# Optimization experiments

Measured on AMD Instinct MI355X. Metric: run time of the kernel, lower is better.

Reference implementation:

```python
import jax, jax.numpy as jnp
import numpy as np

N, E, D, H, L = 20000, 320000, 128, 8, 3
C = D // H  # per-head channels = 16


def setup_inputs() -> dict:
    key = jax.random.key(0)
    ks = jax.random.split(key, 20)
    s = 1.0 / np.sqrt(D)
    inp = {
        "x": jax.random.normal(ks[0], (N, D), dtype=jnp.float32),
        "edge_index": jax.random.randint(ks[1], (2, E), 0, N, dtype=jnp.int64),
        "Wq": jax.random.normal(ks[2], (L, D, D), dtype=jnp.float32) * s,
        "bq": jnp.zeros((L, D), dtype=jnp.float32),
        "Wk": jax.random.normal(ks[3], (L, D, D), dtype=jnp.float32) * s,
        "bk": jnp.zeros((L, D), dtype=jnp.float32),
        "Wv": jax.random.normal(ks[4], (L, D, D), dtype=jnp.float32) * s,
        "bv": jnp.zeros((L, D), dtype=jnp.float32),
        "Wskip": jax.random.normal(ks[5], (L, D, D), dtype=jnp.float32) * s,
        "bskip": jnp.zeros((L, D), dtype=jnp.float32),
        "Wbeta": jax.random.normal(ks[6], (L, 3 * D, 1), dtype=jnp.float32) * (1.0 / np.sqrt(3 * D)),
        "ln_g": jnp.ones((L, D), dtype=jnp.float32),
        "ln_b": jnp.zeros((L, D), dtype=jnp.float32),
        "Wout": jax.random.normal(ks[7], (D, D), dtype=jnp.float32) * s,
        "bout": jnp.zeros((D,), dtype=jnp.float32),
    }
    return inp


def _layer_norm(x, g, b, eps=1e-5):
    mu = jnp.mean(x, axis=-1, keepdims=True)
    var = jnp.mean(jnp.square(x - mu), axis=-1, keepdims=True)
    return (x - mu) * jax.lax.rsqrt(var + eps) * g + b


def _transformer_conv(x, src, dst, Wq, bq, Wk, bk, Wv, bv, Wskip, bskip, Wbeta):
    # project q/k/v: [N, D] -> [N, H, C]
    q = (x @ Wq + bq).reshape(N, H, C)
    k = (x @ Wk + bk).reshape(N, H, C)
    v = (x @ Wv + bv).reshape(N, H, C)
    # per-edge attention logits: [E, H]
    alpha = jnp.sum(q[dst] * k[src], axis=-1) / np.sqrt(C)
    # scatter-softmax over edges grouped by dst node
    m = jax.ops.segment_max(alpha, dst, num_segments=N)  # [N, H]
    m = jnp.where(jnp.isfinite(m), m, 0.0)
    ea = jnp.exp(alpha - m[dst])
    denom = jax.ops.segment_sum(ea, dst, num_segments=N)  # [N, H]
    attn = ea / (denom[dst] + 1e-16)  # [E, H]
    # weighted message aggregation: [N, H, C] -> [N, D]
    out = jax.ops.segment_sum(attn[:, :, None] * v[src], dst, num_segments=N)
    out = out.reshape(N, D)
    # beta-gated skip connection (beta=True, root_weight=True)
    x_r = x @ Wskip + bskip
    beta = jax.nn.sigmoid(jnp.concatenate([out, x_r, out - x_r], axis=-1) @ Wbeta)  # [N, 1]
    return beta * x_r + (1.0 - beta) * out


def reference(x, edge_index, Wq, bq, Wk, bk, Wv, bv, Wskip, bskip, Wbeta, ln_g, ln_b, Wout, bout):
    src, dst = edge_index[0], edge_index[1]
    for i in range(L):
        residual = x
        x = _transformer_conv(x, src, dst, Wq[i], bq[i], Wk[i], bk[i], Wv[i], bv[i],
                              Wskip[i], bskip[i], Wbeta[i])
        x = jax.nn.relu(x)  # dropout is identity in eval mode
        x = _layer_norm(x + residual, ln_g[i], ln_b[i])
    return x @ Wout + bout
```

## Files before the change

### kernel.cpp

```cpp
#include <hip/hip_runtime.h>

#define N_NODES 20000
#define N_EDGES 320000
#define DIM 128
#define NLAYER 3
#define SCAN_BLK 1024
#define N_SCAN_BLKS ((N_NODES + SCAN_BLK - 1) / SCAN_BLK)

typedef __attribute__((ext_vector_type(8))) short short8;
typedef __attribute__((ext_vector_type(4))) float f32x4;

__device__ inline ushort f2bf(float f) {
  uint u = __float_as_uint(f);
  uint r = (u + 0x7fffu + ((u >> 16) & 1u)) >> 16;
  return (ushort)r;
}
__device__ inline float bf2f(ushort u) { return __uint_as_float(((uint)u) << 16); }


__global__ void zero_ints_kernel(int* __restrict__ p, int n) {
  int i = blockIdx.x * 256 + threadIdx.x;
  if (i < n) p[i] = 0;
}

__global__ void count_deg_kernel(const int* __restrict__ ei, int* __restrict__ deg) {
  int e = blockIdx.x * 256 + threadIdx.x;
  if (e < N_EDGES) atomicAdd(&deg[ei[N_EDGES + e]], 1);
}

__global__ __launch_bounds__(SCAN_BLK) void scan1_kernel(const int* __restrict__ deg,
                                                         int* __restrict__ rowptr,
                                                         int* __restrict__ blksum) {
  __shared__ int wsum[16];
  int t = threadIdx.x, lane = t & 63, w = t >> 6;
  int i = blockIdx.x * SCAN_BLK + t;
  int val = (i < N_NODES) ? deg[i] : 0;
  int s = val;
  #pragma unroll
  for (int off = 1; off < 64; off <<= 1) {
    int u = __shfl_up(s, off);
    if (lane >= off) s += u;
  }
  if (lane == 63) wsum[w] = s;
  __syncthreads();
  if (t < 16) {
    int wv = wsum[t];
    int ss = wv;
    #pragma unroll
    for (int off = 1; off < 16; off <<= 1) {
      int u = __shfl_up(ss, off);
      if (t >= off) ss += u;
    }
    wsum[t] = ss - wv;
  }
  __syncthreads();
  int excl = wsum[w] + s - val;
  if (i < N_NODES) rowptr[i] = excl;
  if (t == SCAN_BLK - 1) blksum[blockIdx.x] = excl + val;
}

__global__ void scan2_kernel(int* __restrict__ blksum, int* __restrict__ rowptr) {
  int t = threadIdx.x;
  int val = (t < N_SCAN_BLKS) ? blksum[t] : 0;
  int s = val;
  #pragma unroll
  for (int off = 1; off < 64; off <<= 1) {
    int u = __shfl_up(s, off);
    if (t >= off) s += u;
  }
  if (t < N_SCAN_BLKS) blksum[t] = s - val;
  if (t == 63) rowptr[N_NODES] = s;
}

__global__ __launch_bounds__(SCAN_BLK) void scan3_kernel(int* __restrict__ rowptr,
                                                         const int* __restrict__ blksum) {
  int i = blockIdx.x * SCAN_BLK + threadIdx.x;
  if (i < N_NODES) rowptr[i] += blksum[blockIdx.x];
}

__global__ void scatter_kernel(const int* __restrict__ ei, const int* __restrict__ rowptr,
                               int* __restrict__ cursor, int* __restrict__ csr_src) {
  int e = blockIdx.x * 256 + threadIdx.x;
  if (e < N_EDGES) {
    int d = ei[N_EDGES + e];
    int s = ei[e];
    int pos = atomicAdd(&cursor[d], 1);
    csr_src[rowptr[d] + pos] = s;
  }
}


__global__ void cast_x_kernel(const float* __restrict__ x, ushort* __restrict__ xb, int n4) {
  int i = blockIdx.x * 256 + threadIdx.x;
  if (i < n4) {
    float4 f = ((const float4*)x)[i];
    ushort4 o;
    o.x = f2bf(f.x); o.y = f2bf(f.y); o.z = f2bf(f.z); o.w = f2bf(f.w);
    ((ushort4*)xb)[i] = o;
  }
}

__global__ void cast_w_kernel(const float* __restrict__ Wq, const float* __restrict__ Wk,
                              const float* __restrict__ Wv, const float* __restrict__ Ws,
                              const float* __restrict__ Wo, ushort* __restrict__ wt) {
  int z = blockIdx.z;
  const float* src;
  if (z < 12) {
    int l = z >> 2, j = z & 3;
    src = (j == 0 ? Wq : j == 1 ? Wk : j == 2 ? Wv : Ws) + (size_t)l * DIM * DIM;
  } else {
    src = Wo;
  }
  __shared__ float tile[32][33];
  int tx = threadIdx.x, ty = threadIdx.y;
  int k0 = blockIdx.x * 32, n0 = blockIdx.y * 32;
  #pragma unroll
  for (int i = 0; i < 32; i += 8)
    tile[ty + i][tx] = src[(size_t)(k0 + ty + i) * DIM + n0 + tx];
  __syncthreads();
  ushort* dst = wt + (size_t)z * DIM * DIM;
  #pragma unroll
  for (int i = 0; i < 32; i += 8)
    dst[(size_t)(n0 + ty + i) * DIM + k0 + tx] = f2bf(tile[tx][ty + i]);
}

template <int OUT_BF16>
__global__ __launch_bounds__(256) void gemm_mfma_kernel(
    const ushort* __restrict__ X, const ushort* __restrict__ WT,
    const float* __restrict__ B0, const float* __restrict__ B1,
    const float* __restrict__ B2, const float* __restrict__ B3,
    void* __restrict__ O0, void* __restrict__ O1, void* __restrict__ O2,
    void* __restrict__ O3) {
  int mat = blockIdx.y;
  const ushort* Wt = WT + (size_t)mat * DIM * DIM;
  const float* bias;
  void* O;
  switch (mat) {
    case 0: bias = B0; O = O0; break;
    case 1: bias = B1; O = O1; break;
    case 2: bias = B2; O = O2; break;
    default: bias = B3; O = O3; break;
  }
  int t = threadIdx.x;
  int wid = t >> 6, lane = t & 63;
  int row0 = blockIdx.x * 64 + (wid >> 1) * 32;
  int col0 = (wid & 1) * 64;
  int lr = lane & 15;
  int kc = (lane >> 4) * 8;

  f32x4 acc[2][4];
  #pragma unroll
  for (int i = 0; i < 2; ++i)
    #pragma unroll
    for (int j = 0; j < 4; ++j) acc[i][j] = (f32x4){0.f, 0.f, 0.f, 0.f};

  #pragma unroll
  for (int kb = 0; kb < DIM; kb += 32) {
    short8 a[2], b[4];
    #pragma unroll
    for (int rf = 0; rf < 2; ++rf) {
      int r = row0 + rf * 16 + lr;
      r = min(r, N_NODES - 1);
      a[rf] = *(const short8*)(X + (size_t)r * DIM + kb + kc);
    }
    #pragma unroll
    for (int cf = 0; cf < 4; ++cf) {
      int c = col0 + cf * 16 + lr;
      b[cf] = *(const short8*)(Wt + (size_t)c * DIM + kb + kc);
    }
    #pragma unroll
    for (int rf = 0; rf < 2; ++rf)
      #pragma unroll
      for (int cf = 0; cf < 4; ++cf)
        acc[rf][cf] = __builtin_amdgcn_mfma_f32_16x16x32_bf16(a[rf], b[cf], acc[rf][cf], 0, 0, 0);
  }

  #pragma unroll
  for (int cf = 0; cf < 4; ++cf) {
    int c = col0 + cf * 16 + lr;
    float bv = bias[c];
    #pragma unroll
    for (int rf = 0; rf < 2; ++rf) {
      #pragma unroll
      for (int reg = 0; reg < 4; ++reg) {
        int r = row0 + rf * 16 + (lane >> 4) * 4 + reg;
        if (r < N_NODES) {
          float val = acc[rf][cf][reg] + bv;
          if (OUT_BF16)
            ((ushort*)O)[(size_t)r * DIM + c] = f2bf(val);
          else
            ((float*)O)[(size_t)r * DIM + c] = val;
        }
      }
    }
  }
}

__global__ __launch_bounds__(64) void attn_fused_kernel(
    const ushort* __restrict__ q, const ushort* __restrict__ k, const ushort* __restrict__ v,
    const ushort* __restrict__ xr, const float* __restrict__ xres,
    const int* __restrict__ rowptr, const int* __restrict__ csr_src,
    const float* __restrict__ wbeta, const float* __restrict__ lng,
    const float* __restrict__ lnb, float* __restrict__ xnext,
    ushort* __restrict__ xnextb) {
  __shared__ float lds_s[8][20];
  int n = blockIdx.x;
  int lane = threadIdx.x;
  int h = lane & 7, e = lane >> 3;

  const ushort* qrow = q + (size_t)n * DIM + h * 16;
  short8 q0 = *(const short8*)qrow;
  short8 q1 = *(const short8*)(qrow + 8);
  float qf[16];
  #pragma unroll
  for (int i = 0; i < 8; ++i) {
    qf[i] = bf2f((ushort)q0[i]);
    qf[8 + i] = bf2f((ushort)q1[i]);
  }

  int s0 = rowptr[n];
  int deg = rowptr[n + 1] - s0;
  float acc[16];
  #pragma unroll
  for (int i = 0; i < 16; ++i) acc[i] = 0.f;
  float dsum = 0.f;

  for (int base = 0; base < deg; base += 8) {
    int idx = base + e;
    bool valid = idx < deg;
    int src = csr_src[s0 + min(idx, deg - 1)];
    const ushort* kr = k + (size_t)src * DIM + h * 16;
    const ushort* vr = v + (size_t)src * DIM + h * 16;
    short8 ka = *(const short8*)kr;
    short8 kb2 = *(const short8*)(kr + 8);
    short8 va = *(const short8*)vr;
    short8 vb2 = *(const short8*)(vr + 8);
    float p0 = 0.f, p1 = 0.f;
    #pragma unroll
    for (int i = 0; i < 8; ++i) {
      p0 = fmaf(qf[i], bf2f((ushort)ka[i]), p0);
      p1 = fmaf(qf[8 + i], bf2f((ushort)kb2[i]), p1);
    }
    float ea = __expf((p0 + p1) * 0.25f);
    ea = valid ? ea : 0.f;
    dsum += ea;
    #pragma unroll
    for (int i = 0; i < 8; ++i) {
      acc[i] = fmaf(ea, bf2f((ushort)va[i]), acc[i]);
      acc[8 + i] = fmaf(ea, bf2f((ushort)vb2[i]), acc[8 + i]);
    }
  }

  #pragma unroll
  for (int off = 8; off <= 32; off <<= 1) {
    dsum += __shfl_xor(dsum, off);
    #pragma unroll
    for (int i = 0; i < 16; ++i) acc[i] += __shfl_xor(acc[i], off);
  }
  if (lane < 8) {
    #pragma unroll
    for (int i = 0; i < 16; i += 4)
      *(float4*)&lds_s[lane][i] = make_float4(acc[i], acc[i + 1], acc[i + 2], acc[i + 3]);
    lds_s[lane][16] = dsum;
  }
  __syncthreads();

  int c0 = lane * 2;
  int hh = lane >> 3, cc = (lane & 7) * 2;
  float2 ov = *(float2*)&lds_s[hh][cc];
  float den = lds_s[hh][16];
  float inv = 1.f / (den + 1e-16f);
  float o0 = ov.x * inv, o1 = ov.y * inv;

  ushort2 xru = *(const ushort2*)(xr + (size_t)n * DIM + c0);
  float xr0 = bf2f(xru.x), xr1 = bf2f(xru.y);
  float wa0 = wbeta[c0] + wbeta[2 * DIM + c0];
  float wa1 = wbeta[c0 + 1] + wbeta[2 * DIM + c0 + 1];
  float wb0 = wbeta[DIM + c0] - wbeta[2 * DIM + c0];
  float wb1 = wbeta[DIM + c0 + 1] - wbeta[2 * DIM + c0 + 1];
  float bs = o0 * wa0 + o1 * wa1 + xr0 * wb0 + xr1 * wb1;
  #pragma unroll
  for (int off = 1; off < 64; off <<= 1) bs += __shfl_xor(bs, off);
  float beta = 1.f / (1.f + __expf(-bs));
  float y0 = fmaxf(beta * xr0 + (1.f - beta) * o0, 0.f);
  float y1 = fmaxf(beta * xr1 + (1.f - beta) * o1, 0.f);
  float2 rv = *(const float2*)(xres + (size_t)n * DIM + c0);
  y0 += rv.x;
  y1 += rv.y;
  float s = y0 + y1;
  #pragma unroll
  for (int off = 1; off < 64; off <<= 1) s += __shfl_xor(s, off);
  float mu = s * (1.f / 128.f);
  float d0 = y0 - mu, d1 = y1 - mu;
  float vs = d0 * d0 + d1 * d1;
  #pragma unroll
  for (int off = 1; off < 64; off <<= 1) vs += __shfl_xor(vs, off);
  float rstd = rsqrtf(vs * (1.f / 128.f) + 1e-5f);
  float2 g = *(const float2*)(lng + c0);
  float2 b = *(const float2*)(lnb + c0);
  float out0 = d0 * rstd * g.x + b.x;
  float out1 = d1 * rstd * g.y + b.y;
  *(float2*)(xnext + (size_t)n * DIM + c0) = make_float2(out0, out1);
  ushort2 ob;
  ob.x = f2bf(out0);
  ob.y = f2bf(out1);
  *(ushort2*)(xnextb + (size_t)n * DIM + c0) = ob;
}


extern "C" void kernel_launch(void* const* d_in, const int* in_sizes, int n_in,
                              void* d_out, int out_size, void* d_ws, size_t ws_size,
                              hipStream_t stream) {
  const float* x_in = (const float*)d_in[0];
  const int* ei = (const int*)d_in[1];
  const float* Wq = (const float*)d_in[2];
  const float* bq = (const float*)d_in[3];
  const float* Wk = (const float*)d_in[4];
  const float* bk = (const float*)d_in[5];
  const float* Wv = (const float*)d_in[6];
  const float* bv = (const float*)d_in[7];
  const float* Wsk = (const float*)d_in[8];
  const float* bsk = (const float*)d_in[9];
  const float* Wb = (const float*)d_in[10];
  const float* lng = (const float*)d_in[11];
  const float* lnb = (const float*)d_in[12];
  const float* Wout = (const float*)d_in[13];
  const float* bout = (const float*)d_in[14];
  float* out = (float*)d_out;

  char* p = (char*)d_ws;
  auto alloc = [&](size_t bytes) {
    char* r = p;
    p += (bytes + 255) & ~(size_t)255;
    return r;
  };
  const size_t NB2 = (size_t)N_NODES * DIM * 2;
  const size_t NB4 = (size_t)N_NODES * DIM * 4;
  ushort* xbb = (ushort*)alloc(NB2);
  ushort* qb = (ushort*)alloc(NB2);
  ushort* kb = (ushort*)alloc(NB2);
  ushort* vb = (ushort*)alloc(NB2);
  ushort* xrb = (ushort*)alloc(NB2);
  float* xf0 = (float*)alloc(NB4);
  float* xf1 = (float*)alloc(NB4);
  ushort* wt = (ushort*)alloc((size_t)13 * DIM * DIM * 2);
  int* rowptr = (int*)alloc((N_NODES + 1) * 4);
  int* degc = (int*)alloc(N_NODES * 4);
  int* blksum = (int*)alloc(64 * 4);
  int* csr_src = (int*)alloc(N_EDGES * 4);

  zero_ints_kernel<<<(N_NODES + 255) / 256, 256, 0, stream>>>(degc, N_NODES);
  count_deg_kernel<<<(N_EDGES + 255) / 256, 256, 0, stream>>>(ei, degc);
  scan1_kernel<<<N_SCAN_BLKS, SCAN_BLK, 0, stream>>>(degc, rowptr, blksum);
  scan2_kernel<<<1, 64, 0, stream>>>(blksum, rowptr);
  scan3_kernel<<<N_SCAN_BLKS, SCAN_BLK, 0, stream>>>(rowptr, blksum);
  zero_ints_kernel<<<(N_NODES + 255) / 256, 256, 0, stream>>>(degc, N_NODES);
  scatter_kernel<<<(N_EDGES + 255) / 256, 256, 0, stream>>>(ei, rowptr, degc, csr_src);

  cast_x_kernel<<<(N_NODES * DIM / 4 + 255) / 256, 256, 0, stream>>>(x_in, xbb,
                                                                     N_NODES * DIM / 4);
  cast_w_kernel<<<dim3(4, 4, 13), dim3(32, 8), 0, stream>>>(Wq, Wk, Wv, Wsk, Wout, wt);

  const int GX = (N_NODES + 63) / 64;
  const float* xres = x_in;
  float* xfbufs[NLAYER] = {xf0, xf1, xf0};
  for (int l = 0; l < NLAYER; ++l) {
    gemm_mfma_kernel<1><<<dim3(GX, 4), 256, 0, stream>>>(
        xbb, wt + (size_t)l * 4 * DIM * DIM,
        bq + (size_t)l * DIM, bk + (size_t)l * DIM, bv + (size_t)l * DIM,
        bsk + (size_t)l * DIM, qb, kb, vb, xrb);
    attn_fused_kernel<<<N_NODES, 64, 0, stream>>>(
        qb, kb, vb, xrb, xres, rowptr, csr_src,
        Wb + (size_t)l * 3 * DIM, lng + (size_t)l * DIM, lnb + (size_t)l * DIM,
        xfbufs[l], xbb);
    xres = xfbufs[l];
  }
  gemm_mfma_kernel<0><<<dim3(GX, 1), 256, 0, stream>>>(
      xbb, wt + (size_t)12 * DIM * DIM, bout, bout, bout, bout, out, out, out, out);
}
```

Baseline: 240.8 us.

## Stage X tiles in LDS with 128-row GEMM blocks; fold degree reset into scan

The projection GEMM now loads a 128-row tile of X into padded shared memory once per block. Each wave computes a 64x64 output tile, reading A fragments from LDS instead of re-reading global memory. This halves the grid size and raises per-wave accumulator register use. Separately, zeroing the degree cursor moves into scan3, which removes one kernel launch.

```diff
diff --git a/kernel.cpp b/kernel.cpp
--- a/kernel.cpp
+++ b/kernel.cpp
@@ -6,6 +6,7 @@
 #define NLAYER 3
 #define SCAN_BLK 1024
 #define N_SCAN_BLKS ((N_NODES + SCAN_BLK - 1) / SCAN_BLK)
+#define LDS_STRIDE 136
 
 typedef __attribute__((ext_vector_type(8))) short short8;
 typedef __attribute__((ext_vector_type(4))) float f32x4;
@@ -73,9 +74,13 @@
 }
 
 __global__ __launch_bounds__(SCAN_BLK) void scan3_kernel(int* __restrict__ rowptr,
-                                                         const int* __restrict__ blksum) {
+                                                         const int* __restrict__ blksum,
+                                                         int* __restrict__ degc) {
   int i = blockIdx.x * SCAN_BLK + threadIdx.x;
-  if (i < N_NODES) rowptr[i] += blksum[blockIdx.x];
+  if (i < N_NODES) {
+    rowptr[i] += blksum[blockIdx.x];
+    degc[i] = 0;
+  }
 }
 
 __global__ void scatter_kernel(const int* __restrict__ ei, const int* __restrict__ rowptr,
@@ -131,6 +136,7 @@
     const float* __restrict__ B2, const float* __restrict__ B3,
     void* __restrict__ O0, void* __restrict__ O1, void* __restrict__ O2,
     void* __restrict__ O3) {
+  __shared__ ushort As[128 * LDS_STRIDE];
   int mat = blockIdx.y;
   const ushort* Wt = WT + (size_t)mat * DIM * DIM;
   const float* bias;
@@ -143,47 +149,57 @@
   }
   int t = threadIdx.x;
   int wid = t >> 6, lane = t & 63;
-  int row0 = blockIdx.x * 64 + (wid >> 1) * 32;
-  int col0 = (wid & 1) * 64;
+  int row0 = blockIdx.x * 128;
+  int wr = wid >> 1, wc = wid & 1;
   int lr = lane & 15;
-  int kc = (lane >> 4) * 8;
-
-  f32x4 acc[2][4];
-  #pragma unroll
-  for (int i = 0; i < 2; ++i)
+  int kc8 = (lane >> 4) * 8;
+
+  {
+    int rowi = t >> 4;
+    int col = (t & 15) * 8;
+    #pragma unroll
+    for (int pass = 0; pass < 8; ++pass) {
+      int row = pass * 16 + rowi;
+      int gr = min(row0 + row, N_NODES - 1);
+      short8 val = *(const short8*)(X + (size_t)gr * DIM + col);
+      *(short8*)(As + row * LDS_STRIDE + col) = val;
+    }
+  }
+  __syncthreads();
+
+  f32x4 acc[4][4];
+  #pragma unroll
+  for (int i = 0; i < 4; ++i)
     #pragma unroll
     for (int j = 0; j < 4; ++j) acc[i][j] = (f32x4){0.f, 0.f, 0.f, 0.f};
 
   #pragma unroll
-  for (int kb = 0; kb < DIM; kb += 32) {
-    short8 a[2], b[4];
-    #pragma unroll
-    for (int rf = 0; rf < 2; ++rf) {
-      int r = row0 + rf * 16 + lr;
-      r = min(r, N_NODES - 1);
-      a[rf] = *(const short8*)(X + (size_t)r * DIM + kb + kc);
-    }
+  for (int ks = 0; ks < 4; ++ks) {
+    short8 b[4];
     #pragma unroll
     for (int cf = 0; cf < 4; ++cf) {
-      int c = col0 + cf * 16 + lr;
-      b[cf] = *(const short8*)(Wt + (size_t)c * DIM + kb + kc);
-    }
-    #pragma unroll
-    for (int rf = 0; rf < 2; ++rf)
+      int c = wc * 64 + cf * 16 + lr;
+      b[cf] = *(const short8*)(Wt + (size_t)c * DIM + ks * 32 + kc8);
+    }
+    #pragma unroll
+    for (int rf = 0; rf < 4; ++rf) {
+      int r = wr * 64 + rf * 16 + lr;
+      short8 a = *(const short8*)(As + r * LDS_STRIDE + ks * 32 + kc8);
       #pragma unroll
       for (int cf = 0; cf < 4; ++cf)
-        acc[rf][cf] = __builtin_amdgcn_mfma_f32_16x16x32_bf16(a[rf], b[cf], acc[rf][cf], 0, 0, 0);
+        acc[rf][cf] = __builtin_amdgcn_mfma_f32_16x16x32_bf16(a, b[cf], acc[rf][cf], 0, 0, 0);
+    }
   }
 
   #pragma unroll
   for (int cf = 0; cf < 4; ++cf) {
-    int c = col0 + cf * 16 + lr;
+    int c = wc * 64 + cf * 16 + lr;
     float bv = bias[c];
     #pragma unroll
-    for (int rf = 0; rf < 2; ++rf) {
+    for (int rf = 0; rf < 4; ++rf) {
       #pragma unroll
       for (int reg = 0; reg < 4; ++reg) {
-        int r = row0 + rf * 16 + (lane >> 4) * 4 + reg;
+        int r = row0 + wr * 64 + rf * 16 + (lane >> 4) * 4 + reg;
         if (r < N_NODES) {
           float val = acc[rf][cf][reg] + bv;
           if (OUT_BF16)
@@ -353,15 +369,14 @@
   count_deg_kernel<<<(N_EDGES + 255) / 256, 256, 0, stream>>>(ei, degc);
   scan1_kernel<<<N_SCAN_BLKS, SCAN_BLK, 0, stream>>>(degc, rowptr, blksum);
   scan2_kernel<<<1, 64, 0, stream>>>(blksum, rowptr);
-  scan3_kernel<<<N_SCAN_BLKS, SCAN_BLK, 0, stream>>>(rowptr, blksum);
-  zero_ints_kernel<<<(N_NODES + 255) / 256, 256, 0, stream>>>(degc, N_NODES);
+  scan3_kernel<<<N_SCAN_BLKS, SCAN_BLK, 0, stream>>>(rowptr, blksum, degc);
   scatter_kernel<<<(N_EDGES + 255) / 256, 256, 0, stream>>>(ei, rowptr, degc, csr_src);
 
   cast_x_kernel<<<(N_NODES * DIM / 4 + 255) / 256, 256, 0, stream>>>(x_in, xbb,
                                                                      N_NODES * DIM / 4);
   cast_w_kernel<<<dim3(4, 4, 13), dim3(32, 8), 0, stream>>>(Wq, Wk, Wv, Wsk, Wout, wt);
 
-  const int GX = (N_NODES + 63) / 64;
+  const int GX = (N_NODES + 127) / 128;
   const float* xres = x_in;
   float* xfbufs[NLAYER] = {xf0, xf1, xf0};
   for (int l = 0; l < NLAYER; ++l) {
```

Measured after the change: 218.1 us. 1.1x faster.
